# Performance work log

Hardware: AMD Instinct MI355X
Metric: run time of the kernel (lower is better)

## Reference

```python
import jax, jax.numpy as jnp
import numpy as np

TEMP = 8.0  # softmax temperature from softmax_(X, N=8.0)
EPS = 1e-12  # F.normalize eps


def qmul(q, r):
    # Hamilton product, quaternions stored as (w, x, y, z); broadcasts over leading dims.
    w1, x1, y1, z1 = q[..., 0], q[..., 1], q[..., 2], q[..., 3]
    w2, x2, y2, z2 = r[..., 0], r[..., 1], r[..., 2], r[..., 3]
    return jnp.stack([
        w1 * w2 - x1 * x2 - y1 * y2 - z1 * z2,
        w1 * x2 + x1 * w2 + y1 * z2 - z1 * y2,
        w1 * y2 - x1 * z2 + y1 * w2 + z1 * x2,
        w1 * z2 + x1 * y2 - y1 * x2 + z1 * w2,
    ], axis=-1)


def setup_inputs() -> dict:
    key = jax.random.key(0)
    kl, kq, krq, kw, ks, kd = jax.random.split(key, 6)
    N, K, E = 100000, 8, 3200000
    node_levels = jax.random.uniform(kl, (N, K), dtype=jnp.float32)
    node_q = jax.random.normal(kq, (N, K, 4), dtype=jnp.float32)
    node_q = node_q / jnp.linalg.norm(node_q, axis=-1, keepdims=True)
    edge_rel_q = jax.random.normal(krq, (E, 4), dtype=jnp.float32)
    edge_rel_q = edge_rel_q / jnp.linalg.norm(edge_rel_q, axis=-1, keepdims=True)
    edge_w = jax.random.uniform(kw, (E,), dtype=jnp.float32)
    edge_src = jax.random.randint(ks, (E,), 0, N, dtype=jnp.int32)
    edge_dst = jax.random.randint(kd, (E,), 0, N, dtype=jnp.int32)
    return {"node_levels": node_levels, "node_q": node_q, "edge_rel_q": edge_rel_q,
            "edge_w": edge_w, "edge_src": edge_src, "edge_dst": edge_dst}


def reference(node_levels, node_q, edge_rel_q, edge_w, edge_src, edge_dst):
    N, K = node_levels.shape
    # --- gather (DGL message_func): per-edge source features ---
    q_src = node_q[edge_src]          # [E,K,4]
    l_src = node_levels[edge_src]     # [E,K]
    # accumulated quaternion: rel_q (broadcast over K) * neighbor q
    accu_q = qmul(edge_rel_q[:, None, :], q_src)  # [E,K,4]

    # --- distance-weighted softmax over {self} U in-neighbors, per (node, k) ---
    score_e = TEMP * edge_w[:, None] * l_src      # [E,K]  edge term: w * l
    score_s = TEMP * node_levels                  # [N,K]  self term: w=1
    seg_max = jax.ops.segment_max(score_e, edge_dst, num_segments=N)  # -inf if no in-edges
    m = jnp.maximum(seg_max, score_s)             # [N,K] stable max incl. self
    exp_e = jnp.exp(score_e - m[edge_dst])
    exp_s = jnp.exp(score_s - m)
    denom = jax.ops.segment_sum(exp_e, edge_dst, num_segments=N) + exp_s  # [N,K]
    w_e = exp_e / denom[edge_dst]                 # [E,K]
    w_s = exp_s / denom                           # [N,K]

    # --- weighted aggregation (scatter) ---
    out_q = jax.ops.segment_sum(w_e[..., None] * accu_q, edge_dst, num_segments=N) \
            + w_s[..., None] * node_q             # [N,K,4]
    out_levels = jax.ops.segment_sum(w_e * l_src, edge_dst, num_segments=N) \
            + w_s * node_levels                   # [N,K]

    # F.normalize(p=2, dim=-1) with eps clamp
    norm = jnp.maximum(jnp.linalg.norm(out_q, axis=-1, keepdims=True), EPS)
    q = out_q / norm
    return q, out_levels
```

## Files before the change

### kernel.cpp

```cpp
#include <hip/hip_runtime.h>
#include <hip/hip_fp16.h>

#define TEMP 8.0f
#define MSHIFT 8.0f
#define KDIM 8
#define BKT_SHIFT 7
#define BKT_NODES (1 << BKT_SHIFT)
#define MAXNB 1024
#define TILE 3072
#define PTHR 512
#define EPT 6
#define BPT 2
#define EPB_H 8192
#define CAPB 4736

__device__ __forceinline__ unsigned pack_h2(float a, float b) {
    __half2 h = __floats2half2_rn(a, b);
    return __builtin_bit_cast(unsigned, h);
}
__device__ __forceinline__ float2 unpack_h2(unsigned v) {
    __half2 h = __builtin_bit_cast(__half2, v);
    return __half22float2(h);
}

__device__ __forceinline__ unsigned long long pack_ql(float4 q, float l) {
    int lu = __float2int_rn(l * 4095.0f);
    lu = lu < 0 ? 0 : (lu > 4095 ? 4095 : lu);
    int vw = __float2int_rn(q.x * 4095.0f);
    int vx = __float2int_rn(q.y * 4095.0f);
    int vy = __float2int_rn(q.z * 4095.0f);
    int vz = __float2int_rn(q.w * 4095.0f);
    return (unsigned long long)(unsigned)lu
         | ((unsigned long long)((unsigned)vw & 0x1FFFu) << 12)
         | ((unsigned long long)((unsigned)vx & 0x1FFFu) << 25)
         | ((unsigned long long)((unsigned)vy & 0x1FFFu) << 38)
         | ((unsigned long long)((unsigned)vz & 0x1FFFu) << 51);
}

__device__ __forceinline__ int sext13(unsigned v) {
    return ((int)(v << 19)) >> 19;
}

__global__ void prep_hist(const float* __restrict__ levels,
                          const float4* __restrict__ node_q,
                          unsigned long long* __restrict__ qltab, int NK, int gN,
                          const int* __restrict__ edst,
                          int* __restrict__ ghist, int E) {
    __shared__ int h[MAXNB];
    if ((int)blockIdx.x < gN) {
        int i = blockIdx.x * blockDim.x + threadIdx.x;
        if (i >= NK) return;
        qltab[i] = pack_ql(node_q[i], levels[i]);
    } else {
        int tid = threadIdx.x;
        for (int i = tid; i < MAXNB; i += 256) h[i] = 0;
        __syncthreads();
        int beg = (blockIdx.x - gN) * EPB_H;
        int end = beg + EPB_H; if (end > E) end = E;
        for (int e = beg + tid; e < end; e += 256)
            atomicAdd(&h[edst[e] >> BKT_SHIFT], 1);
        __syncthreads();
        for (int i = tid; i < MAXNB; i += 256)
            if (h[i]) atomicAdd(&ghist[i], h[i]);
    }
}

__global__ void scan_buckets(const int* __restrict__ ghist,
                             int* __restrict__ gbase,
                             int* __restrict__ gcursor, int NBKT, int E) {
    __shared__ int s[1024];
    __shared__ int carry_s;
    int tid = threadIdx.x;
    if (tid == 0) carry_s = 0;
    __syncthreads();
    for (int base = 0; base < MAXNB; base += 1024) {
        int idx = base + tid;
        int v = (idx < NBKT) ? ghist[idx] : 0;
        s[tid] = v;
        __syncthreads();
        for (int off = 1; off < 1024; off <<= 1) {
            int t = (tid >= off) ? s[tid - off] : 0;
            __syncthreads();
            s[tid] += t;
            __syncthreads();
        }
        if (idx < NBKT) {
            int b = s[tid] - v + carry_s;
            gbase[idx] = b;
            gcursor[idx] = b;
        }
        __syncthreads();
        if (tid == 0) carry_s += s[1023];
        __syncthreads();
    }
    if (tid == 0) gbase[NBKT] = E;
}

__global__ void __launch_bounds__(PTHR, 4)
partition_lds(const int* __restrict__ edst,
              const int* __restrict__ esrc,
              const float* __restrict__ ew,
              const float4* __restrict__ rel_q,
              int* __restrict__ gcursor,
              float4* __restrict__ ebuf,
              unsigned char* __restrict__ dib, int E) {
    __shared__ float4 sortbuf[TILE];
    __shared__ unsigned char sdib[TILE];
    __shared__ unsigned short sbk[TILE];
    __shared__ int cnt[MAXNB];
    __shared__ int base[MAXNB];
    __shared__ int gpos[MAXNB];
    __shared__ int ts[PTHR];

    int tid = threadIdx.x;
    int tbeg = blockIdx.x * TILE;
    int tcnt = E - tbeg; if (tcnt > TILE) tcnt = TILE;

    for (int i = tid; i < MAXNB; i += PTHR) cnt[i] = 0;
    __syncthreads();

    int eb[EPT]; int er[EPT]; unsigned char ed[EPT]; bool ev[EPT];
#pragma unroll
    for (int i = 0; i < EPT; ++i) {
        int e = tbeg + i * PTHR + tid;
        ev[i] = (e < E);
        if (ev[i]) {
            int d = edst[e];
            eb[i] = d >> BKT_SHIFT;
            ed[i] = (unsigned char)(d & (BKT_NODES - 1));
            er[i] = atomicAdd(&cnt[eb[i]], 1);
        }
    }
    __syncthreads();

    int loc = 0;
#pragma unroll
    for (int j = 0; j < BPT; ++j) {
        int b = tid * BPT + j;
        base[b] = loc;
        loc += cnt[b];
    }
    ts[tid] = loc;
    __syncthreads();
    for (int off = 1; off < PTHR; off <<= 1) {
        int t = (tid >= off) ? ts[tid - off] : 0;
        __syncthreads();
        ts[tid] += t;
        __syncthreads();
    }
    int tb = ts[tid] - loc;
#pragma unroll
    for (int j = 0; j < BPT; ++j) base[tid * BPT + j] += tb;
    __syncthreads();

#pragma unroll
    for (int i = 0; i < EPT; ++i) {
        if (ev[i]) {
            int e = tbeg + i * PTHR + tid;
            float4 rq = rel_q[e];
            uint4 u;
            u.x = pack_h2(rq.x, rq.y);
            u.y = pack_h2(rq.z, rq.w);
            u.z = __builtin_bit_cast(unsigned, TEMP * ew[e]);
            u.w = (unsigned)(esrc[e] * KDIM);
            int pos = base[eb[i]] + er[i];
            sortbuf[pos] = __builtin_bit_cast(float4, u);
            sdib[pos] = ed[i];
            sbk[pos] = (unsigned short)eb[i];
        }
    }
    __syncthreads();

    for (int b = tid; b < MAXNB; b += PTHR)
        if (cnt[b]) gpos[b] = atomicAdd(&gcursor[b], cnt[b]);
    __syncthreads();

    for (int pos = tid; pos < tcnt; pos += PTHR) {
        int b = sbk[pos];
        int dst = gpos[b] + (pos - base[b]);
        ebuf[dst] = sortbuf[pos];
        dib[dst] = sdib[pos];
    }
}

__global__ void fine_lds(const int* __restrict__ gbase,
                         const float4* __restrict__ ebuf,
                         const unsigned char* __restrict__ dib,
                         float4* __restrict__ payload,
                         int* __restrict__ deg,
                         int* __restrict__ offs, int N) {
    __shared__ float4 outbuf[CAPB];
    __shared__ int h[BKT_NODES];
    __shared__ int hx[BKT_NODES];
    __shared__ int c[BKT_NODES];
    int bk = blockIdx.x;
    int tid = threadIdx.x;
    int beg = gbase[bk], end = gbase[bk + 1];
    int cnt = end - beg;

    if (tid < BKT_NODES) { h[tid] = 0; c[tid] = 0; }
    __syncthreads();
    for (int s = beg + tid; s < end; s += 256)
        atomicAdd(&h[dib[s]], 1);
    __syncthreads();
    if (tid < BKT_NODES) hx[tid] = h[tid];
    __syncthreads();
    for (int off = 1; off < BKT_NODES; off <<= 1) {
        int t = (tid >= off && tid < BKT_NODES) ? hx[tid - off] : 0;
        __syncthreads();
        if (tid < BKT_NODES) hx[tid] += t;
        __syncthreads();
    }
    if (tid < BKT_NODES) {
        int ex = hx[tid] - h[tid];
        hx[tid] = ex;
        int n = (bk << BKT_SHIFT) + tid;
        if (n < N) { deg[n] = h[tid]; offs[n] = beg + ex; }
    }
    __syncthreads();
    for (int s = beg + tid; s < end; s += 256) {
        int d = dib[s];
        int r = atomicAdd(&c[d], 1);
        int op = hx[d] + r;
        float4 v = ebuf[s];
        if (op < CAPB) outbuf[op] = v;
        else payload[beg + op] = v;
    }
    __syncthreads();
    int lim = cnt < CAPB ? cnt : CAPB;
    for (int s = tid; s < lim; s += 256)
        payload[beg + s] = outbuf[s];
}

__global__ void agg_wave(const float* __restrict__ levels,
                         const float4* __restrict__ node_q,
                         const unsigned long long* __restrict__ qltab,
                         const int* __restrict__ deg,
                         const int* __restrict__ offs,
                         const float4* __restrict__ payload,
                         float4* __restrict__ out_q,
                         float* __restrict__ out_lvl, int N) {
    int t = blockIdx.x * blockDim.x + threadIdx.x;
    int n = t >> 6;
    if (n >= N) return;
    int lane = t & 63;
    int k = lane & 7;
    int seg = lane >> 3;

    const float QS = 1.0f / 4095.0f;
    float den = 0.f, lv = 0.f, aw = 0.f, ax = 0.f, ay = 0.f, az = 0.f;

    int cnt = deg[n];
    const float4* bp = payload + offs[n];

    for (int j0 = seg; j0 < cnt; j0 += 48) {
        float4 pe[6];
        bool v[6];
#pragma unroll
        for (int s = 0; s < 6; ++s) {
            int j = j0 + s * 8;
            v[s] = (j < cnt);
            if (v[s]) pe[s] = bp[j];
        }
        unsigned long long g[6];
#pragma unroll
        for (int s = 0; s < 6; ++s)
            if (v[s])
                g[s] = qltab[(int)__builtin_bit_cast(uint4, pe[s]).w + k];
#pragma unroll
        for (int s = 0; s < 6; ++s)
            if (v[s]) {
                uint4 pu = __builtin_bit_cast(uint4, pe[s]);
                float2 r01 = unpack_h2(pu.x);
                float2 r23 = unpack_h2(pu.y);
                float tw = __builtin_bit_cast(float, pu.z);
                unsigned long long p = g[s];
                float ls = (float)(unsigned)(p & 0xFFFu) * QS;
                float qw = (float)sext13((unsigned)((p >> 12) & 0x1FFFu)) * QS;
                float qx = (float)sext13((unsigned)((p >> 25) & 0x1FFFu)) * QS;
                float qy = (float)sext13((unsigned)((p >> 38) & 0x1FFFu)) * QS;
                float qz = (float)sext13((unsigned)((p >> 51) & 0x1FFFu)) * QS;
                float ex = __expf(tw * ls - MSHIFT);
                den += ex;
                lv += ex * ls;
                float rw = r01.x, rx = r01.y, ry = r23.x, rz = r23.y;
                aw += ex * (rw * qw - rx * qx - ry * qy - rz * qz);
                ax += ex * (rw * qx + rx * qw + ry * qz - rz * qy);
                ay += ex * (rw * qy - rx * qz + ry * qw + rz * qx);
                az += ex * (rw * qz + rx * qy - ry * qx + rz * qw);
            }
    }

#pragma unroll
    for (int m = 8; m <= 32; m <<= 1) {
        den += __shfl_xor(den, m, 64);
        lv  += __shfl_xor(lv,  m, 64);
        aw  += __shfl_xor(aw,  m, 64);
        ax  += __shfl_xor(ax,  m, 64);
        ay  += __shfl_xor(ay,  m, 64);
        az  += __shfl_xor(az,  m, 64);
    }

    if (seg == 0) {
        int i = n * KDIM + k;
        float l = levels[i];
        float es = __expf(TEMP * l - MSHIFT);
        den += es;
        lv += es * l;
        float4 q0 = node_q[i];
        aw += es * q0.x; ax += es * q0.y; ay += es * q0.z; az += es * q0.w;

        float inv = 1.0f / den;
        lv *= inv; aw *= inv; ax *= inv; ay *= inv; az *= inv;
        float nn = sqrtf(aw * aw + ax * ax + ay * ay + az * az);
        nn = fmaxf(nn, 1e-12f);
        float rn = 1.0f / nn;
        float4 o;
        o.x = aw * rn; o.y = ax * rn; o.z = ay * rn; o.w = az * rn;
        out_q[i] = o;
        out_lvl[i] = lv;
    }
}


__global__ void rank_kernel(const int* __restrict__ edst, int* __restrict__ deg,
                            int* __restrict__ rank, int E) {
    int e = blockIdx.x * blockDim.x + threadIdx.x;
    if (e < E) rank[e] = atomicAdd(&deg[edst[e]], 1);
}

__global__ void scan1(const int* __restrict__ deg, int* __restrict__ offs,
                      int* __restrict__ bsum, int N) {
    __shared__ int s[256];
    int i = blockIdx.x * 256 + threadIdx.x;
    int v = (i < N) ? deg[i] : 0;
    s[threadIdx.x] = v;
    __syncthreads();
    for (int off = 1; off < 256; off <<= 1) {
        int t = (threadIdx.x >= off) ? s[threadIdx.x - off] : 0;
        __syncthreads();
        s[threadIdx.x] += t;
        __syncthreads();
    }
    if (i < N) offs[i] = s[threadIdx.x] - v;
    if (threadIdx.x == 255) bsum[blockIdx.x] = s[255];
}

__global__ void scan2(int* __restrict__ bsum, int nb) {
    __shared__ int s[1024];
    __shared__ int carry_s;
    if (threadIdx.x == 0) carry_s = 0;
    __syncthreads();
    for (int base = 0; base < nb; base += 1024) {
        int idx = base + threadIdx.x;
        int v = (idx < nb) ? bsum[idx] : 0;
        s[threadIdx.x] = v;
        __syncthreads();
        for (int off = 1; off < 1024; off <<= 1) {
            int t = (threadIdx.x >= off) ? s[threadIdx.x - off] : 0;
            __syncthreads();
            s[threadIdx.x] += t;
            __syncthreads();
        }
        if (idx < nb) bsum[idx] = s[threadIdx.x] - v + carry_s;
        __syncthreads();
        if (threadIdx.x == 0) carry_s += s[1023];
        __syncthreads();
    }
}

__global__ void scan3(int* __restrict__ offs, const int* __restrict__ bsum,
                      int N, int E) {
    int i = blockIdx.x * 256 + threadIdx.x;
    if (i < N) offs[i] += bsum[blockIdx.x];
    if (i == 0) offs[N] = E;
}

__global__ void permute_kernel(const int* __restrict__ edst,
                               const int* __restrict__ rank,
                               const int* __restrict__ offs,
                               const float4* __restrict__ rel_q,
                               const float* __restrict__ ew,
                               const int* __restrict__ esrc,
                               float4* __restrict__ payload, int E) {
    int e = blockIdx.x * blockDim.x + threadIdx.x;
    if (e >= E) return;
    int pos = offs[edst[e]] + rank[e];
    payload[2 * pos] = rel_q[e];
    float4 m;
    m.x = TEMP * ew[e];
    m.y = __int_as_float(esrc[e] * KDIM);
    m.z = 0.0f; m.w = 0.0f;
    payload[2 * pos + 1] = m;
}

__global__ void agg_payload(const float* __restrict__ levels,
                            const float4* __restrict__ node_q,
                            const int* __restrict__ offs,
                            const float4* __restrict__ payload,
                            float4* __restrict__ out_q,
                            float* __restrict__ out_lvl, int N) {
    int t = blockIdx.x * blockDim.x + threadIdx.x;
    int n = t >> 3;
    int k = t & 7;
    if (n >= N) return;
    int i = n * KDIM + k;
    float l = levels[i];
    float es = __expf(TEMP * l - MSHIFT);
    float den = es, lv = es * l;
    float4 q0 = node_q[i];
    float aw = es * q0.x, ax = es * q0.y, ay = es * q0.z, az = es * q0.w;
    int beg = offs[n], end = offs[n + 1];
#pragma unroll 2
    for (int j = beg; j < end; j++) {
        float4 r = payload[2 * j];
        float4 m = payload[2 * j + 1];
        float tw = m.x;
        int src8 = __float_as_int(m.y);
        float ls = levels[src8 + k];
        float ex = __expf(tw * ls - MSHIFT);
        float4 q = node_q[src8 + k];
        den += ex;
        lv += ex * ls;
        aw += ex * (r.x * q.x - r.y * q.y - r.z * q.z - r.w * q.w);
        ax += ex * (r.x * q.y + r.y * q.x + r.z * q.w - r.w * q.z);
        ay += ex * (r.x * q.z - r.y * q.w + r.z * q.x + r.w * q.y);
        az += ex * (r.x * q.w + r.y * q.z - r.z * q.y + r.w * q.x);
    }
    float inv = 1.0f / den;
    lv *= inv; aw *= inv; ax *= inv; ay *= inv; az *= inv;
    float nn = sqrtf(aw * aw + ax * ax + ay * ay + az * az);
    nn = fmaxf(nn, 1e-12f);
    float rn = 1.0f / nn;
    float4 o;
    o.x = aw * rn; o.y = ax * rn; o.z = ay * rn; o.w = az * rn;
    out_q[i] = o;
    out_lvl[i] = lv;
}

extern "C" void kernel_launch(void* const* d_in, const int* in_sizes, int n_in,
                              void* d_out, int out_size, void* d_ws, size_t ws_size,
                              hipStream_t stream) {
    const float*  levels = (const float*)d_in[0];
    const float4* node_q = (const float4*)d_in[1];
    const float4* rel_q  = (const float4*)d_in[2];
    const float*  ew     = (const float*)d_in[3];
    const int*    esrc   = (const int*)d_in[4];
    const int*    edst   = (const int*)d_in[5];

    const int NK = in_sizes[0];
    const int E  = in_sizes[3];
    const int N  = NK / KDIM;
    const int B  = 256;
    const int gE = (E + B - 1) / B;
    const int gN = (NK + B - 1) / B;

    float* out_q   = (float*)d_out;
    float* out_lvl = (float*)d_out + (size_t)NK * 4;

    const int NBKT = (N + BKT_NODES - 1) >> BKT_SHIFT;
    const int HB   = (E + EPB_H - 1) / EPB_H;
    auto al = [](size_t x) { return (x + 255) & ~(size_t)255; };
    size_t o_ghist = 0;
    size_t o_gbase = o_ghist + al((size_t)MAXNB * 4);
    size_t o_gcur  = o_gbase + al((size_t)(MAXNB + 1) * 4);
    size_t o_deg   = o_gcur  + al((size_t)MAXNB * 4);
    size_t o_offs  = o_deg   + al((size_t)N * 4);
    size_t o_qltab = o_offs  + al((size_t)N * 4);
    size_t o_dib   = o_qltab + al((size_t)NK * 8);
    size_t o_ebuf  = o_dib   + al((size_t)E);
    size_t o_pay   = o_ebuf  + al((size_t)E * 16);
    size_t need    = o_pay   + al((size_t)E * 16);

    if (NBKT <= MAXNB && ws_size >= need) {
        int* ghist   = (int*)((char*)d_ws + o_ghist);
        int* gbase   = (int*)((char*)d_ws + o_gbase);
        int* gcursor = (int*)((char*)d_ws + o_gcur);
        int* deg     = (int*)((char*)d_ws + o_deg);
        int* offs    = (int*)((char*)d_ws + o_offs);
        unsigned long long* qltab = (unsigned long long*)((char*)d_ws + o_qltab);
        unsigned char* dib = (unsigned char*)((char*)d_ws + o_dib);
        float4* ebuf    = (float4*)((char*)d_ws + o_ebuf);
        float4* payload = (float4*)((char*)d_ws + o_pay);

        (void)hipMemsetAsync(ghist, 0, (size_t)MAXNB * 4, stream);
        prep_hist<<<gN + HB, B, 0, stream>>>(levels, node_q, qltab, NK, gN,
                                             edst, ghist, E);
        scan_buckets<<<1, 1024, 0, stream>>>(ghist, gbase, gcursor, NBKT, E);
        int PB = (E + TILE - 1) / TILE;
        partition_lds<<<PB, PTHR, 0, stream>>>(edst, esrc, ew, rel_q, gcursor,
                                               ebuf, dib, E);
        fine_lds<<<NBKT, B, 0, stream>>>(gbase, ebuf, dib, payload, deg, offs, N);
        int gW = (int)(((size_t)N * 64 + B - 1) / B);
        agg_wave<<<gW, B, 0, stream>>>(levels, node_q, qltab, deg, offs,
                                       payload, (float4*)out_q, out_lvl, N);
        return;
    }

    const int nb = (N + 255) / 256;
    int* deg  = (int*)d_ws;
    int* offs = deg + N;
    int* bsum = offs + N + 1;
    size_t prefix = (size_t)(2 * N + 1 + nb);
    int* rank = bsum + nb;
    size_t pay_off = (prefix + E + 3) & ~(size_t)3;
    float4* payload = (float4*)((int*)d_ws + pay_off);

    (void)hipMemsetAsync(deg, 0, (size_t)N * sizeof(int), stream);
    rank_kernel<<<gE, B, 0, stream>>>(edst, deg, rank, E);
    scan1<<<nb, 256, 0, stream>>>(deg, offs, bsum, N);
    scan2<<<1, 1024, 0, stream>>>(bsum, nb);
    scan3<<<nb, 256, 0, stream>>>(offs, bsum, N, E);
    permute_kernel<<<gE, B, 0, stream>>>(edst, rank, offs, rel_q, ew, esrc,
                                         payload, E);
    agg_payload<<<gN, B, 0, stream>>>(levels, node_q, offs, payload,
                                      (float4*)out_q, out_lvl, N);
}
```

Before: 310.2 us.

## Fuse fine bucket sort into aggregation using LDS atomic accumulation per bucket

Removes the fine per-node sort kernel and the separate per-node aggregation. The destination-in-bucket index is packed into the upper bits of the source word, and one block per 128-node bucket accumulates softmax numerators and denominators into shared memory with float atomics. This drops a full pass that read and wrote the 16-byte-per-edge payload, plus the dib byte array. In exchange it adds six LDS atomics per edge, and with only about 782 buckets there is reduced parallelism and a risk of atomic contention. The new guard condition on N also looks odd.

```diff
diff --git a/kernel.cpp b/kernel.cpp
--- a/kernel.cpp
+++ b/kernel.cpp
@@ -12,7 +12,7 @@
 #define EPT 6
 #define BPT 2
 #define EPB_H 8192
-#define CAPB 4736
+#define SRC_MASK 0x7FFFFFu
 
 __device__ __forceinline__ unsigned pack_h2(float a, float b) {
     __half2 h = __floats2half2_rn(a, b);
@@ -102,10 +102,8 @@
               const float* __restrict__ ew,
               const float4* __restrict__ rel_q,
               int* __restrict__ gcursor,
-              float4* __restrict__ ebuf,
-              unsigned char* __restrict__ dib, int E) {
+              float4* __restrict__ ebuf, int E) {
     __shared__ float4 sortbuf[TILE];
-    __shared__ unsigned char sdib[TILE];
     __shared__ unsigned short sbk[TILE];
     __shared__ int cnt[MAXNB];
     __shared__ int base[MAXNB];
@@ -162,10 +160,9 @@
             u.x = pack_h2(rq.x, rq.y);
             u.y = pack_h2(rq.z, rq.w);
             u.z = __builtin_bit_cast(unsigned, TEMP * ew[e]);
-            u.w = (unsigned)(esrc[e] * KDIM);
+            u.w = (unsigned)(esrc[e] * KDIM) | ((unsigned)ed[i] << 23);
             int pos = base[eb[i]] + er[i];
             sortbuf[pos] = __builtin_bit_cast(float4, u);
-            sdib[pos] = ed[i];
             sbk[pos] = (unsigned short)eb[i];
         }
     }
@@ -177,96 +174,46 @@
 
     for (int pos = tid; pos < tcnt; pos += PTHR) {
         int b = sbk[pos];
-        int dst = gpos[b] + (pos - base[b]);
-        ebuf[dst] = sortbuf[pos];
-        dib[dst] = sdib[pos];
-    }
-}
-
-__global__ void fine_lds(const int* __restrict__ gbase,
-                         const float4* __restrict__ ebuf,
-                         const unsigned char* __restrict__ dib,
-                         float4* __restrict__ payload,
-                         int* __restrict__ deg,
-                         int* __restrict__ offs, int N) {
-    __shared__ float4 outbuf[CAPB];
-    __shared__ int h[BKT_NODES];
-    __shared__ int hx[BKT_NODES];
-    __shared__ int c[BKT_NODES];
+        ebuf[gpos[b] + (pos - base[b])] = sortbuf[pos];
+    }
+}
+
+__global__ void __launch_bounds__(256, 4)
+agg_bucket(const float* __restrict__ levels,
+           const float4* __restrict__ node_q,
+           const unsigned long long* __restrict__ qltab,
+           const int* __restrict__ gbase,
+           const float4* __restrict__ ebuf,
+           float4* __restrict__ out_q,
+           float* __restrict__ out_lvl, int N) {
+    __shared__ float acc[BKT_NODES * KDIM * 6];
     int bk = blockIdx.x;
     int tid = threadIdx.x;
     int beg = gbase[bk], end = gbase[bk + 1];
-    int cnt = end - beg;
-
-    if (tid < BKT_NODES) { h[tid] = 0; c[tid] = 0; }
-    __syncthreads();
-    for (int s = beg + tid; s < end; s += 256)
-        atomicAdd(&h[dib[s]], 1);
-    __syncthreads();
-    if (tid < BKT_NODES) hx[tid] = h[tid];
-    __syncthreads();
-    for (int off = 1; off < BKT_NODES; off <<= 1) {
-        int t = (tid >= off && tid < BKT_NODES) ? hx[tid - off] : 0;
-        __syncthreads();
-        if (tid < BKT_NODES) hx[tid] += t;
-        __syncthreads();
-    }
-    if (tid < BKT_NODES) {
-        int ex = hx[tid] - h[tid];
-        hx[tid] = ex;
-        int n = (bk << BKT_SHIFT) + tid;
-        if (n < N) { deg[n] = h[tid]; offs[n] = beg + ex; }
-    }
-    __syncthreads();
-    for (int s = beg + tid; s < end; s += 256) {
-        int d = dib[s];
-        int r = atomicAdd(&c[d], 1);
-        int op = hx[d] + r;
-        float4 v = ebuf[s];
-        if (op < CAPB) outbuf[op] = v;
-        else payload[beg + op] = v;
-    }
-    __syncthreads();
-    int lim = cnt < CAPB ? cnt : CAPB;
-    for (int s = tid; s < lim; s += 256)
-        payload[beg + s] = outbuf[s];
-}
-
-__global__ void agg_wave(const float* __restrict__ levels,
-                         const float4* __restrict__ node_q,
-                         const unsigned long long* __restrict__ qltab,
-                         const int* __restrict__ deg,
-                         const int* __restrict__ offs,
-                         const float4* __restrict__ payload,
-                         float4* __restrict__ out_q,
-                         float* __restrict__ out_lvl, int N) {
-    int t = blockIdx.x * blockDim.x + threadIdx.x;
-    int n = t >> 6;
-    if (n >= N) return;
-    int lane = t & 63;
-    int k = lane & 7;
-    int seg = lane >> 3;
-
+
+    for (int i = tid; i < BKT_NODES * KDIM * 6; i += 256) acc[i] = 0.f;
+    __syncthreads();
+
+    int k = tid & 7;
+    int seg = tid >> 3;
     const float QS = 1.0f / 4095.0f;
-    float den = 0.f, lv = 0.f, aw = 0.f, ax = 0.f, ay = 0.f, az = 0.f;
-
-    int cnt = deg[n];
-    const float4* bp = payload + offs[n];
-
-    for (int j0 = seg; j0 < cnt; j0 += 48) {
+
+    for (int j0 = beg + seg; j0 < end; j0 += 32 * 6) {
         float4 pe[6];
         bool v[6];
 #pragma unroll
         for (int s = 0; s < 6; ++s) {
-            int j = j0 + s * 8;
-            v[s] = (j < cnt);
-            if (v[s]) pe[s] = bp[j];
+            int j = j0 + s * 32;
+            v[s] = (j < end);
+            if (v[s]) pe[s] = ebuf[j];
         }
         unsigned long long g[6];
 #pragma unroll
         for (int s = 0; s < 6; ++s)
-            if (v[s])
-                g[s] = qltab[(int)__builtin_bit_cast(uint4, pe[s]).w + k];
+            if (v[s]) {
+                unsigned w = __builtin_bit_cast(uint4, pe[s]).w;
+                g[s] = qltab[(int)(w & SRC_MASK) + k];
+            }
 #pragma unroll
         for (int s = 0; s < 6; ++s)
             if (v[s]) {
@@ -274,6 +221,7 @@
                 float2 r01 = unpack_h2(pu.x);
                 float2 r23 = unpack_h2(pu.y);
                 float tw = __builtin_bit_cast(float, pu.z);
+                int dib = (int)(pu.w >> 23);
                 unsigned long long p = g[s];
                 float ls = (float)(unsigned)(p & 0xFFFu) * QS;
                 float qw = (float)sext13((unsigned)((p >> 12) & 0x1FFFu)) * QS;
@@ -281,35 +229,32 @@
                 float qy = (float)sext13((unsigned)((p >> 38) & 0x1FFFu)) * QS;
                 float qz = (float)sext13((unsigned)((p >> 51) & 0x1FFFu)) * QS;
                 float ex = __expf(tw * ls - MSHIFT);
-                den += ex;
-                lv += ex * ls;
                 float rw = r01.x, rx = r01.y, ry = r23.x, rz = r23.y;
-                aw += ex * (rw * qw - rx * qx - ry * qy - rz * qz);
-                ax += ex * (rw * qx + rx * qw + ry * qz - rz * qy);
-                ay += ex * (rw * qy - rx * qz + ry * qw + rz * qx);
-                az += ex * (rw * qz + rx * qy - ry * qx + rz * qw);
+                float* a = &acc[(dib * KDIM + k) * 6];
+                atomicAdd(a + 0, ex);
+                atomicAdd(a + 1, ex * ls);
+                atomicAdd(a + 2, ex * (rw * qw - rx * qx - ry * qy - rz * qz));
+                atomicAdd(a + 3, ex * (rw * qx + rx * qw + ry * qz - rz * qy));
+                atomicAdd(a + 4, ex * (rw * qy - rx * qz + ry * qw + rz * qx));
+                atomicAdd(a + 5, ex * (rw * qz + rx * qy - ry * qx + rz * qw));
             }
     }
-
-#pragma unroll
-    for (int m = 8; m <= 32; m <<= 1) {
-        den += __shfl_xor(den, m, 64);
-        lv  += __shfl_xor(lv,  m, 64);
-        aw  += __shfl_xor(aw,  m, 64);
-        ax  += __shfl_xor(ax,  m, 64);
-        ay  += __shfl_xor(ay,  m, 64);
-        az  += __shfl_xor(az,  m, 64);
-    }
-
-    if (seg == 0) {
-        int i = n * KDIM + k;
+    __syncthreads();
+
+    int base_n = bk << BKT_SHIFT;
+    for (int t = tid; t < BKT_NODES * KDIM; t += 256) {
+        int node = t >> 3, kk = t & 7;
+        int n = base_n + node;
+        if (n >= N) continue;
+        const float* a = &acc[t * 6];
+        float den = a[0], lv = a[1], aw = a[2], ax = a[3], ay = a[4], az = a[5];
+        int i = n * KDIM + kk;
         float l = levels[i];
         float es = __expf(TEMP * l - MSHIFT);
         den += es;
         lv += es * l;
         float4 q0 = node_q[i];
         aw += es * q0.x; ax += es * q0.y; ay += es * q0.z; az += es * q0.w;
-
         float inv = 1.0f / den;
         lv *= inv; aw *= inv; ax *= inv; ay *= inv; az *= inv;
         float nn = sqrtf(aw * aw + ax * ax + ay * ay + az * az);
@@ -464,24 +409,16 @@
     size_t o_ghist = 0;
     size_t o_gbase = o_ghist + al((size_t)MAXNB * 4);
     size_t o_gcur  = o_gbase + al((size_t)(MAXNB + 1) * 4);
-    size_t o_deg   = o_gcur  + al((size_t)MAXNB * 4);
-    size_t o_offs  = o_deg   + al((size_t)N * 4);
-    size_t o_qltab = o_offs  + al((size_t)N * 4);
-    size_t o_dib   = o_qltab + al((size_t)NK * 8);
-    size_t o_ebuf  = o_dib   + al((size_t)E);
-    size_t o_pay   = o_ebuf  + al((size_t)E * 16);
-    size_t need    = o_pay   + al((size_t)E * 16);
-
-    if (NBKT <= MAXNB && ws_size >= need) {
+    size_t o_qltab = o_gcur  + al((size_t)MAXNB * 4);
+    size_t o_ebuf  = o_qltab + al((size_t)NK * 8);
+    size_t need    = o_ebuf  + al((size_t)E * 16);
+
+    if (NBKT <= MAXNB && ws_size >= need && N < (1 << 20) / KDIM * 8) {
         int* ghist   = (int*)((char*)d_ws + o_ghist);
         int* gbase   = (int*)((char*)d_ws + o_gbase);
         int* gcursor = (int*)((char*)d_ws + o_gcur);
-        int* deg     = (int*)((char*)d_ws + o_deg);
-        int* offs    = (int*)((char*)d_ws + o_offs);
         unsigned long long* qltab = (unsigned long long*)((char*)d_ws + o_qltab);
-        unsigned char* dib = (unsigned char*)((char*)d_ws + o_dib);
-        float4* ebuf    = (float4*)((char*)d_ws + o_ebuf);
-        float4* payload = (float4*)((char*)d_ws + o_pay);
+        float4* ebuf = (float4*)((char*)d_ws + o_ebuf);
 
         (void)hipMemsetAsync(ghist, 0, (size_t)MAXNB * 4, stream);
         prep_hist<<<gN + HB, B, 0, stream>>>(levels, node_q, qltab, NK, gN,
@@ -489,11 +426,9 @@
         scan_buckets<<<1, 1024, 0, stream>>>(ghist, gbase, gcursor, NBKT, E);
         int PB = (E + TILE - 1) / TILE;
         partition_lds<<<PB, PTHR, 0, stream>>>(edst, esrc, ew, rel_q, gcursor,
-                                               ebuf, dib, E);
-        fine_lds<<<NBKT, B, 0, stream>>>(gbase, ebuf, dib, payload, deg, offs, N);
-        int gW = (int)(((size_t)N * 64 + B - 1) / B);
-        agg_wave<<<gW, B, 0, stream>>>(levels, node_q, qltab, deg, offs,
-                                       payload, (float4*)out_q, out_lvl, N);
+                                               ebuf, E);
+        agg_bucket<<<NBKT, B, 0, stream>>>(levels, node_q, qltab, gbase, ebuf,
+                                           (float4*)out_q, out_lvl, N);
         return;
     }
 
```

Measured after the change: 1.205 ms. +288.4%, slower.
